# Optimization experiments

Hardware: AMD Instinct MI355X
Metric: run time of the kernel (lower is better)

Reference implementation:

```python
import jax, jax.numpy as jnp
import numpy as np
import math

B = 1024      # graphs
N = 64        # nodes per graph (padded, masked by node_mask)
BN = B * N    # total nodes
EPG = 192     # directed edges per graph
E = B * EPG


def setup_inputs() -> dict:
    key = jax.random.key(0)
    ks = jax.random.split(key, 40)

    def nrm(k, shp, s=0.02):
        return (jax.random.normal(k, shp) * s).astype(jnp.float32)

    mol_batch_x = jax.random.normal(ks[0], (BN, 19), dtype=jnp.float32)
    offs = jnp.arange(B, dtype=jnp.int32) * N
    src = jax.random.randint(ks[1], (B, EPG), 0, N, dtype=jnp.int32) + offs[:, None]
    dst = jax.random.randint(ks[2], (B, EPG), 0, N, dtype=jnp.int32) + offs[:, None]
    mol_batch_edge_index = jnp.stack([src.reshape(-1), dst.reshape(-1)], axis=0)
    mol_batch_batch = jnp.repeat(jnp.arange(B, dtype=jnp.int32), N)
    text_features = jax.random.normal(ks[3], (B, 300), dtype=jnp.float32)
    timesteps = jax.random.uniform(ks[4], (B,), minval=0.0, maxval=1000.0, dtype=jnp.float32)
    node_mask = (jax.random.uniform(ks[5], (B, N)) > 0.1).astype(jnp.float32)

    p = {
        'W_tr': nrm(ks[6], (19, 300)),   'b_tr': jnp.zeros((300,), jnp.float32),
        'W_c1': nrm(ks[7], (300, 600)),  'b_c1': jnp.zeros((600,), jnp.float32),
        'W_c2': nrm(ks[8], (600, 600)),  'b_c2': jnp.zeros((600,), jnp.float32),
        'W_c3': nrm(ks[9], (600, 600)),  'b_c3': jnp.zeros((600,), jnp.float32),
        'W_h1': nrm(ks[10], (600, 600)), 'b_h1': jnp.zeros((600,), jnp.float32),
        'W_h2': nrm(ks[11], (600, 600)), 'b_h2': jnp.zeros((600,), jnp.float32),
        'W_h3': nrm(ks[12], (600, 300)), 'b_h3': jnp.zeros((300,), jnp.float32),
        'ln_g': jnp.ones((300,), jnp.float32), 'ln_b': jnp.zeros((300,), jnp.float32),
        'W_t1': nrm(ks[13], (128, 512)), 'b_t1': jnp.zeros((512,), jnp.float32),
        'W_t2': nrm(ks[14], (512, 512)), 'b_t2': jnp.zeros((512,), jnp.float32),
        'W_e':  nrm(ks[15], (512, 3000)), 'b_e': jnp.zeros((3000,), jnp.float32),
    }
    return dict(mol_batch_x=mol_batch_x, mol_batch_edge_index=mol_batch_edge_index,
                mol_batch_batch=mol_batch_batch, text_features=text_features,
                timesteps=timesteps, node_mask=node_mask, **p)


def timestep_embedding(t, dim=128, max_period=10000.0):
    half = dim // 2
    freqs = jnp.exp(-math.log(max_period) * jnp.arange(half, dtype=jnp.float32) / half)
    args = t[:, None] * freqs[None]                 # [B, half]
    return jnp.concatenate([jnp.cos(args), jnp.sin(args)], axis=-1)  # [B, dim]


def gcn_conv(x, W, b, src, dst, num_nodes):
    # PyG GCNConv: D^{-1/2} (A + I) D^{-1/2} X W + b, edge weights 1
    h = x @ W                                             # [BN, F]
    deg = jnp.zeros((num_nodes,), h.dtype).at[dst].add(1.0) + 1.0  # in-degree + self-loop
    inv_sqrt = jax.lax.rsqrt(deg)
    coef = inv_sqrt[src] * inv_sqrt[dst]                  # [E]
    agg = jax.ops.segment_sum(h[src] * coef[:, None], dst, num_segments=num_nodes)
    return agg + h * (1.0 / deg)[:, None] + b             # self-loop norm = 1/deg


def global_mean_pool(x, batch, num_graphs):
    sums = jax.ops.segment_sum(x, batch, num_segments=num_graphs)
    cnts = jax.ops.segment_sum(jnp.ones((x.shape[0],), x.dtype), batch, num_segments=num_graphs)
    return sums / jnp.maximum(cnts, 1.0)[:, None]


def layer_norm(x, g, b, eps=1e-5):
    mu = jnp.mean(x, axis=-1, keepdims=True)
    var = jnp.mean(jnp.square(x - mu), axis=-1, keepdims=True)
    return (x - mu) * jax.lax.rsqrt(var + eps) * g + b


def reference(mol_batch_x, mol_batch_edge_index, mol_batch_batch, text_features,
              timesteps, node_mask, W_tr, b_tr, W_c1, b_c1, W_c2, b_c2, W_c3, b_c3,
              W_h1, b_h1, W_h2, b_h2, W_h3, b_h3, ln_g, ln_b,
              W_t1, b_t1, W_t2, b_t2, W_e, b_e):
    num_nodes = mol_batch_x.shape[0]
    num_graphs = node_mask.shape[0]
    src, dst = mol_batch_edge_index[0], mol_batch_edge_index[1]

    # FiLM conditioning from timestep embedding
    emb = jax.nn.relu(timestep_embedding(timesteps, 128) @ W_t1 + b_t1) @ W_t2 + b_t2  # [B,512]
    emb_out = jax.nn.relu(emb) @ W_e + b_e                                             # [B,3000]
    s1, t1 = emb_out[:, 0:600], emb_out[:, 600:1200]
    s2, t2 = emb_out[:, 1200:1800], emb_out[:, 1800:2400]
    s3, t3 = emb_out[:, 2400:2700], emb_out[:, 2700:3000]

    # node transform + mask
    x = mol_batch_x @ W_tr + b_tr                     # [BN, 300]
    x = x * node_mask.reshape(-1, 1)

    # GCN stack
    x = jax.nn.relu(gcn_conv(x, W_c1, b_c1, src, dst, num_nodes))
    x = jax.nn.relu(gcn_conv(x, W_c2, b_c2, src, dst, num_nodes))
    x = gcn_conv(x, W_c3, b_c3, src, dst, num_nodes)  # [BN, 600]

    g = global_mean_pool(x, mol_batch_batch, num_graphs)  # [B, 600]
    g = jax.nn.relu(g @ W_h1 + b_h1)
    g = g * (1.0 + s1) + t1
    g = jax.nn.relu(g @ W_h2 + b_h2)
    g = g * (1.0 + s2) + t2
    g = g @ W_h3 + b_h3                                # [B, 300]
    g = g * (1.0 + s3) + t3
    g = layer_norm(g, ln_g, ln_b)
    return (g, text_features)
```

## Files before the change

### kernel.cpp

```cpp
#include <hip/hip_runtime.h>
#include <hip/hip_bf16.h>
#include <cstdint>
#include <cstddef>

static constexpr int B   = 1024;
static constexpr int N   = 64;
static constexpr int BN  = B * N;
static constexpr int EPG = 192;
static constexpr int E   = B * EPG;
static constexpr int FP  = 608;
static constexpr int KP1 = 320;
static constexpr int PMS = 80;
static constexpr int NCONV = 2560;

typedef __hip_bfloat16 bf16;
typedef __bf16 bf16x8 __attribute__((ext_vector_type(8)));
typedef __bf16 bf16x4 __attribute__((ext_vector_type(4)));
typedef float  f32x4  __attribute__((ext_vector_type(4)));

__device__ __forceinline__ void storeC(float* p, float v) { *p = v; }
__device__ __forceinline__ void storeC(bf16* p, float v) { *p = __float2bfloat16(v); }

__device__ __forceinline__ void llds16(const void* g, void* l) {
    __builtin_amdgcn_global_load_lds(
        (const __attribute__((address_space(1))) unsigned int*)g,
        (__attribute__((address_space(3))) unsigned int*)l,
        16, 0, 0);
}

template<bool RELU, bool FILM, typename CT>
__device__ __forceinline__ void g64_tile(
    const bf16* __restrict__ A, int lda,
    const bf16* __restrict__ Bt, int ldb,
    const float* __restrict__ bias,
    CT* __restrict__ C, int ldc, int Ncap,
    const bf16* __restrict__ fS, const bf16* __restrict__ fT, int fstride,
    int K, int m0, int n0, __bf16* As, __bf16* Bs, int tid)
{
    const int lane = tid & 63;
    const int w    = tid >> 6;
    const int wn   = w * 32;
    const int l15  = lane & 15;
    const int lhi  = lane >> 4;

    f32x4 acc[4][2] = {};

    for (int k0 = 0; k0 < K; k0 += 32) {
        {
            int row = tid >> 2, kc = tid & 3;
            char* la = (char*)As + (size_t)(w * 64) * 16;
            llds16(A + (size_t)(m0 + row) * lda + k0 + kc * 8, la);
        }
        #pragma unroll
        for (int t = 0; t < 2; ++t) {
            int ci  = t * 256 + tid;
            int row = ci >> 2, kc = ci & 3;
            char* lb = (char*)Bs + (size_t)(t * 256 + w * 64) * 16;
            llds16(Bt + (size_t)(n0 + row) * ldb + k0 + kc * 8, lb);
        }
        asm volatile("s_waitcnt vmcnt(0)" ::: "memory");
        __syncthreads();

        bf16x8 af[4], bg[2];
        #pragma unroll
        for (int i = 0; i < 4; ++i)
            af[i] = *(bf16x8*)(As + (i * 16 + l15) * 32 + lhi * 8);
        #pragma unroll
        for (int j = 0; j < 2; ++j)
            bg[j] = *(bf16x8*)(Bs + (wn + j * 16 + l15) * 32 + lhi * 8);
        #pragma unroll
        for (int i = 0; i < 4; ++i)
            #pragma unroll
            for (int j = 0; j < 2; ++j)
                acc[i][j] = __builtin_amdgcn_mfma_f32_16x16x32_bf16(
                    af[i], bg[j], acc[i][j], 0, 0, 0);
        __syncthreads();
    }

    #pragma unroll
    for (int i = 0; i < 4; ++i) {
        #pragma unroll
        for (int j = 0; j < 2; ++j) {
            int col = n0 + wn + j * 16 + l15;
            if (col < Ncap) {
                float bv = bias ? bias[col] : 0.f;
                #pragma unroll
                for (int e = 0; e < 4; ++e) {
                    int row = m0 + i * 16 + lhi * 4 + e;
                    float v = acc[i][j][e] + bv;
                    if (RELU) v = fmaxf(v, 0.f);
                    if (FILM) {
                        float sv = __bfloat162float(fS[(size_t)row * fstride + col]);
                        float tv = __bfloat162float(fT[(size_t)row * fstride + col]);
                        v = v * (1.f + sv) + tv;
                    }
                    storeC(&C[(size_t)row * ldc + col], v);
                }
            }
        }
    }
}

__device__ __attribute__((noinline)) void guest_g64(
    const bf16* gA, int glda, const bf16* gBt, int gldb,
    const float* gbias, bf16* gC, int gldc, int gNcap, int gK, int gnt,
    int t, char* lds, int tid)
{
    int mt2 = t / gnt, nt2 = t % gnt;
    g64_tile<true, false, bf16>(gA, glda, gBt, gldb, gbias, gC, gldc, gNcap,
                                nullptr, nullptr, 0, gK, mt2 * 64, nt2 * 128,
                                (__bf16*)lds, (__bf16*)(lds + 4096), tid);
}

template<bool RELU, bool FILM, typename CT>
__global__ __launch_bounds__(256) void gemm64(
    const bf16* __restrict__ A, int lda,
    const bf16* __restrict__ Bt, int ldb,
    const float* __restrict__ bias,
    CT* __restrict__ C, int ldc, int Ncap,
    const bf16* __restrict__ fS, const bf16* __restrict__ fT, int fstride,
    int K)
{
    __shared__ __align__(16) __bf16 As[64 * 32];
    __shared__ __align__(16) __bf16 Bs[128 * 32];
    g64_tile<RELU, FILM, CT>(A, lda, Bt, ldb, bias, C, ldc, Ncap,
                             fS, fT, fstride, K,
                             blockIdx.x * 64, blockIdx.y * 128, As, Bs,
                             threadIdx.x);
}

__global__ __launch_bounds__(256) void k_two_gemms(
    const bf16* __restrict__ A2b, const bf16* __restrict__ Wet,
    const float* __restrict__ b_e, bf16* __restrict__ EO,
    const bf16* __restrict__ Yv, const bf16* __restrict__ Wb3,
    const float* __restrict__ b_c3, bf16* __restrict__ G0)
{
    __shared__ __align__(16) __bf16 As[64 * 32];
    __shared__ __align__(16) __bf16 Bs[128 * 32];
    int bid = blockIdx.x;
    if (bid < 384) {
        int mt = bid / 24, nt = bid % 24;
        g64_tile<false, false, bf16>(A2b, 512, Wet, 512, b_e, EO, 3000, 3000,
                                     nullptr, nullptr, 0, 512,
                                     mt * 64, nt * 128, As, Bs, threadIdx.x);
    } else {
        int t = bid - 384;
        int mt = t / 5, nt = t % 5;
        g64_tile<false, false, bf16>(Yv, FP, Wb3, FP, b_c3, G0, FP, 600,
                                     nullptr, nullptr, 0, FP,
                                     mt * 64, nt * 128, As, Bs, threadIdx.x);
    }
}

__global__ __launch_bounds__(256) void conv1_gemm(
    const bf16* __restrict__ A,
    const bf16* __restrict__ Bt,
    const float* __restrict__ bias,
    bf16* __restrict__ X1,
    const bf16* __restrict__ gA, int glda,
    const bf16* __restrict__ gBt, int gldb,
    const float* __restrict__ gbias,
    bf16* __restrict__ gC, int gldc, int gNcap, int gK, int gnt)
{
    __shared__ __align__(16) char regA[17408];
    const int tid = threadIdx.x;
    const int bid = blockIdx.x;

    if (bid >= NCONV) {
        guest_g64(gA, glda, gBt, gldb, gbias, gC, gldc, gNcap, gK, gnt,
                  bid - NCONV, regA, tid);
        return;
    }

    __bf16* As = (__bf16*)regA;
    __bf16* Bs = (__bf16*)(regA + 8192);

    const int lane = tid & 63;
    const int w    = tid >> 6;
    const int wm   = (w & 1) * 64;
    const int wn   = (w >> 1) * 64;
    const int l15  = lane & 15;
    const int lhi  = lane >> 4;

    const int lid = bid >> 3;
    const int mt  = (bid & 7) * 64 + lid / 5;
    const int nt  = lid % 5;
    const int m0  = mt * 128;
    const int n0  = nt * 128;

    f32x4 acc[4][4] = {};
    for (int k0 = 0; k0 < KP1; k0 += 32) {
        #pragma unroll
        for (int t = 0; t < 2; ++t) {
            int ci  = t * 256 + w * 64 + lane;
            int row = ci >> 2, kc = ci & 3;
            char* la = (char*)As + (size_t)(t * 256 + w * 64) * 16;
            char* lb = (char*)Bs + (size_t)(t * 256 + w * 64) * 16;
            llds16(A  + (size_t)(m0 + row) * KP1 + k0 + kc * 8, la);
            llds16(Bt + (size_t)(n0 + row) * KP1 + k0 + kc * 8, lb);
        }
        asm volatile("s_waitcnt vmcnt(0)" ::: "memory");
        __syncthreads();

        bf16x8 af[4], bg[4];
        #pragma unroll
        for (int i = 0; i < 4; ++i)
            af[i] = *(bf16x8*)(As + (wm + i * 16 + l15) * 32 + lhi * 8);
        #pragma unroll
        for (int j = 0; j < 4; ++j)
            bg[j] = *(bf16x8*)(Bs + (wn + j * 16 + l15) * 32 + lhi * 8);
        #pragma unroll
        for (int i = 0; i < 4; ++i)
            #pragma unroll
            for (int j = 0; j < 4; ++j)
                acc[i][j] = __builtin_amdgcn_mfma_f32_16x16x32_bf16(
                    af[i], bg[j], acc[i][j], 0, 0, 0);
        __syncthreads();
    }

    #pragma unroll
    for (int i = 0; i < 4; ++i)
        #pragma unroll
        for (int j = 0; j < 4; ++j) {
            int col = n0 + wn + j * 16 + l15;
            if (col < FP) {
                float bv = (col < 600) ? bias[col] : 0.f;
                #pragma unroll
                for (int e = 0; e < 4; ++e) {
                    int row = m0 + wm + i * 16 + lhi * 4 + e;
                    float v = fmaxf(acc[i][j][e] + bv, 0.f);
                    X1[(size_t)row * FP + col] = __float2bfloat16(v);
                }
            }
        }
}

__global__ __launch_bounds__(256) void conv_fused_q(
    const bf16* __restrict__ A, int lda, int K,
    const bf16* __restrict__ Bt, int ldb,
    const bf16* __restrict__ Pmg,
    const float* __restrict__ bias,
    const float* __restrict__ qv,
    bf16* __restrict__ Y,
    const bf16* __restrict__ gA, int glda,
    const bf16* __restrict__ gBt, int gldb,
    const float* __restrict__ gbias,
    bf16* __restrict__ gC, int gldc, int gNcap, int gK, int gnt)
{
    __shared__ __align__(16) char regA[17408];
    __shared__ __align__(16) __bf16 Pm[128 * PMS];
    __shared__ float s_q[128];

    const int tid = threadIdx.x;
    const int bid = blockIdx.x;

    if (bid >= NCONV) {
        guest_g64(gA, glda, gBt, gldb, gbias, gC, gldc, gNcap, gK, gnt,
                  bid - NCONV, regA, tid);
        return;
    }

    __bf16* As = (__bf16*)regA;
    __bf16* Bs = (__bf16*)(regA + 8192);
    __bf16* Ts = (__bf16*)regA;

    const int lane = tid & 63;
    const int w    = tid >> 6;
    const int wm   = (w & 1) * 64;
    const int wn   = (w >> 1) * 64;
    const int l15  = lane & 15;
    const int lhi  = lane >> 4;

    const int lid = bid >> 3;
    const int mt  = (bid & 7) * 64 + lid / 5;
    const int nt  = lid % 5;
    const int m0  = mt * 128;
    const int n0  = nt * 128;

    #pragma unroll
    for (int i = 0; i < 5; ++i) {
        int cbase = w * 320 + i * 64;
        llds16(Pmg + (size_t)mt * (128 * PMS) + (size_t)(cbase + lane) * 8,
               (char*)Pm + (size_t)cbase * 16);
    }
    if (tid < 128) s_q[tid] = qv[mt * 128 + tid];

    f32x4 acc[4][4] = {};
    for (int k0 = 0; k0 < K; k0 += 32) {
        #pragma unroll
        for (int t = 0; t < 2; ++t) {
            int ci  = t * 256 + w * 64 + lane;
            int row = ci >> 2, kc = ci & 3;
            char* la = (char*)As + (size_t)(t * 256 + w * 64) * 16;
            char* lb = (char*)Bs + (size_t)(t * 256 + w * 64) * 16;
            llds16(A  + (size_t)(m0 + row) * lda + k0 + kc * 8, la);
            llds16(Bt + (size_t)(n0 + row) * ldb + k0 + kc * 8, lb);
        }
        asm volatile("s_waitcnt vmcnt(0)" ::: "memory");
        __syncthreads();

        bf16x8 af[4], bg[4];
        #pragma unroll
        for (int i = 0; i < 4; ++i)
            af[i] = *(bf16x8*)(As + (wm + i * 16 + l15) * 32 + lhi * 8);
        #pragma unroll
        for (int j = 0; j < 4; ++j)
            bg[j] = *(bf16x8*)(Bs + (wn + j * 16 + l15) * 32 + lhi * 8);
        #pragma unroll
        for (int i = 0; i < 4; ++i)
            #pragma unroll
            for (int j = 0; j < 4; ++j)
                acc[i][j] = __builtin_amdgcn_mfma_f32_16x16x32_bf16(
                    af[i], bg[j], acc[i][j], 0, 0, 0);
        __syncthreads();
    }

    const int g  = w & 1;
    const int nb = w >> 1;
    #pragma unroll
    for (int h = 0; h < 2; ++h) {
        if (wn == h * 64) {
            #pragma unroll
            for (int i = 0; i < 4; ++i)
                #pragma unroll
                for (int j = 0; j < 4; ++j) {
                    int c_local = j * 16 + l15;
                    int rbase   = wm + i * 16 + lhi * 4;
                    bf16x4 pk;
                    #pragma unroll
                    for (int e = 0; e < 4; ++e) pk[e] = (__bf16)acc[i][j][e];
                    *(bf16x4*)(Ts + c_local * 136 + rbase) = pk;
                }
        }
        __syncthreads();

        f32x4 acc2[4][2] = {};
        #pragma unroll
        for (int k0 = 0; k0 < 64; k0 += 32) {
            bf16x8 pa[4], hb[2];
            #pragma unroll
            for (int i = 0; i < 4; ++i)
                pa[i] = *(bf16x8*)(Pm + (g * 64 + i * 16 + l15) * PMS + k0 + lhi * 8);
            #pragma unroll
            for (int j = 0; j < 2; ++j)
                hb[j] = *(bf16x8*)(Ts + (nb * 32 + j * 16 + l15) * 136
                                      + g * 64 + k0 + lhi * 8);
            #pragma unroll
            for (int i = 0; i < 4; ++i)
                #pragma unroll
                for (int j = 0; j < 2; ++j)
                    acc2[i][j] = __builtin_amdgcn_mfma_f32_16x16x32_bf16(
                        pa[i], hb[j], acc2[i][j], 0, 0, 0);
        }
        #pragma unroll
        for (int j = 0; j < 2; ++j) {
            int col = n0 + h * 64 + nb * 32 + j * 16 + l15;
            float bv = (col < 600) ? bias[col] : 0.f;
            float yp = 0.f;
            #pragma unroll
            for (int i = 0; i < 4; ++i)
                #pragma unroll
                for (int e = 0; e < 4; ++e) {
                    float v = fmaxf(acc2[i][j][e] + bv, 0.f);
                    yp += s_q[g * 64 + i * 16 + lhi * 4 + e] * v;
                }
            yp += __shfl_xor(yp, 16, 64);
            yp += __shfl_xor(yp, 32, 64);
            if (lhi == 0 && col < FP)
                Y[(size_t)(mt * 2 + g) * FP + col] = __float2bfloat16(yp);
        }
        __syncthreads();
    }
}

struct WtJob  { const float* src; bf16* dst; int Ksrc, Nsrc, Kp, Np, blk0; };
struct PrepArgs {
    WtJob j[9];
    int nwt, te0, pp0, xtr0;
    const int*   ei;
    const float* ts;
    const float* xin; const float* Wtr; const float* btr; const float* mask;
    bf16* TE; bf16* Pmg; float* qv; bf16* PX0;
};

__global__ __launch_bounds__(256) void k_prep(PrepArgs a)
{
    __shared__ __align__(16) char sm[35840];
    const int bx  = blockIdx.x;
    const int tid = threadIdx.x;

    if (bx < a.nwt) {
        int ji = 0;
        while (ji < 8 && bx >= a.j[ji + 1].blk0) ++ji;
        WtJob jb = a.j[ji];
        int t  = bx - jb.blk0;
        int kt = (jb.Kp + 63) >> 6;
        int ti = t % kt, tj = t / kt;
        int kg0 = ti * 64, ng0 = tj * 64;
        float (*T)[65] = (float(*)[65])sm;
        #pragma unroll 4
        for (int r = 0; r < 16; ++r) {
            int kl = (tid >> 6) + r * 4, nl = tid & 63;
            int kg = kg0 + kl, ng = ng0 + nl;
            T[kl][nl] = (kg < jb.Ksrc && ng < jb.Nsrc)
                        ? jb.src[(size_t)kg * jb.Nsrc + ng] : 0.f;
        }
        __syncthreads();
        #pragma unroll 4
        for (int r = 0; r < 16; ++r) {
            int nl = (tid >> 6) + r * 4, kl = tid & 63;
            int ng = ng0 + nl, kg = kg0 + kl;
            if (ng < jb.Np && kg < jb.Kp)
                jb.dst[(size_t)ng * jb.Kp + kg] = __float2bfloat16(T[kl][nl]);
        }
    } else if (bx < a.pp0) {
        int idx = (bx - a.te0) * 256 + tid;
        int b = idx >> 7, jj = idx & 127;
        float tt = a.ts[b];
        int h = jj & 63;
        float freq = expf(-9.210340371976184f * (float)h / 64.f);
        float ang = tt * freq;
        a.TE[idx] = __float2bfloat16((jj < 64) ? cosf(ang) : sinf(ang));
    } else if (bx < a.xtr0) {
        int pr = bx - a.pp0;
        float* Pf   = (float*)sm;
        int*   cnt  = (int*)(sm + 32768);
        float* sQ   = (float*)(sm + 33280);
        float* sI   = (float*)(sm + 33792);
        float* sIvd = (float*)(sm + 34304);

        for (int idx = tid; idx < 8192; idx += 256) Pf[idx] = 0.f;
        if (tid < 128) cnt[tid] = 0;
        __syncthreads();
        for (int e = tid; e < 2 * EPG; e += 256) {
            int g  = (e >= EPG);
            int eg = (2 * pr + g) * EPG + (e - g * EPG);
            int ld = (a.ei[E + eg] & 63) + g * 64;
            atomicAdd(&cnt[ld], 1);
        }
        __syncthreads();
        if (tid < 128) {
            float d = (float)cnt[tid] + 1.0f;
            float iv = 1.f / d;
            sIvd[tid] = iv;
            sI[tid]   = rsqrtf(d);
            sQ[tid]   = iv;
        }
        __syncthreads();
        for (int e = tid; e < 2 * EPG; e += 256) {
            int g   = (e >= EPG);
            int eg  = (2 * pr + g) * EPG + (e - g * EPG);
            int lsl = a.ei[eg] & 63;
            int ldl = a.ei[E + eg] & 63;
            float cf = sI[g * 64 + lsl] * sI[g * 64 + ldl];
            atomicAdd(&Pf[(g * 64 + ldl) * 64 + lsl], cf);
            atomicAdd(&sQ[g * 64 + lsl], cf);
        }
        __syncthreads();
        if (tid < 128) {
            Pf[tid * 64 + (tid & 63)] += sIvd[tid];
            a.qv[pr * 128 + tid] = sQ[tid] * (1.f / 64.f);
        }
        __syncthreads();
        for (int idx = tid; idx < 128 * PMS; idx += 256) {
            int r = idx / PMS, k = idx - r * PMS;
            float v = (k < 64) ? Pf[r * 64 + k] : 0.f;
            a.Pmg[(size_t)pr * (128 * PMS) + idx] = __float2bfloat16(v);
        }
    } else {
        int g = bx - a.xtr0;
        float* Pf  = (float*)sm;
        float* Ws  = (float*)sm;
        float* xm  = (float*)(sm + 23104);
        float* xa  = (float*)(sm + 28224);
        float* isqv= (float*)(sm + 33344);
        float* ivdv= (float*)(sm + 33600);
        int*   cnt = (int*)  (sm + 33856);
        float* sb  = (float*)(sm + 34112);

        for (int idx = tid; idx < 4096; idx += 256) Pf[idx] = 0.f;
        if (tid < 64) cnt[tid] = 0;
        __syncthreads();
        for (int e = tid; e < EPG; e += 256)
            atomicAdd(&cnt[a.ei[E + g * EPG + e] & 63], 1);
        __syncthreads();
        if (tid < 64) {
            float d = (float)cnt[tid] + 1.0f;
            ivdv[tid] = 1.f / d;
            isqv[tid] = rsqrtf(d);
        }
        __syncthreads();
        for (int e = tid; e < EPG; e += 256) {
            int ls = a.ei[g * EPG + e] & 63;
            int ld = a.ei[E + g * EPG + e] & 63;
            atomicAdd(&Pf[ld * 64 + ls], isqv[ls] * isqv[ld]);
        }
        for (int idx = tid; idx < 64 * 20; idx += 256) {
            int n = idx / 20, j = idx - n * 20;
            float mv = a.mask[g * 64 + n];
            xm[idx] = (j < 19) ? mv * a.xin[(size_t)(g * 64 + n) * 19 + j] : mv;
        }
        __syncthreads();
        if (tid < 64) Pf[tid * 64 + tid] += ivdv[tid];
        __syncthreads();
        for (int idx = tid; idx < 64 * 20; idx += 256) {
            int r = idx / 20, j = idx - r * 20;
            float s = 0.f;
            #pragma unroll 8
            for (int s2 = 0; s2 < 64; ++s2)
                s += Pf[r * 64 + s2] * xm[s2 * 20 + j];
            xa[idx] = s;
        }
        __syncthreads();
        for (int idx = tid; idx < 19 * 304; idx += 256) {
            int k = idx / 304, c = idx - k * 304;
            Ws[idx] = (c < 300) ? a.Wtr[k * 300 + c] : 0.f;
        }
        for (int c = tid; c < 304; c += 256)
            sb[c] = (c < 300) ? a.btr[c] : 0.f;
        __syncthreads();
        int n  = tid >> 2;
        int c0 = tid & 3;
        float ba = xa[n * 20 + 19];
        for (int c = c0; c < 304; c += 4) {
            float acc = ba * sb[c];
            #pragma unroll
            for (int k = 0; k < 19; ++k)
                acc += xa[n * 20 + k] * Ws[k * 304 + c];
            a.PX0[(size_t)(g * 64 + n) * KP1 + c] = __float2bfloat16(acc);
        }
        bf16x8 z = {};
        for (int idx = tid; idx < 64 * 2; idx += 256) {
            int nn = idx >> 1, jv = idx & 1;
            *(bf16x8*)((__bf16*)a.PX0 + (size_t)(g * 64 + nn) * KP1 + 304 + jv * 8) = z;
        }
    }
}

__global__ __launch_bounds__(256) void k_ln_copy(const float* __restrict__ G,
                                                 const float* __restrict__ lg,
                                                 const float* __restrict__ lb,
                                                 const float* __restrict__ text,
                                                 float* __restrict__ out)
{
    int r = blockIdx.x;
    int tid = threadIdx.x;
    __shared__ float red[4];
    __shared__ float smu, svar;

    float v0 = (tid < 300) ? G[r * 300 + tid] : 0.f;
    float v1 = (tid + 256 < 300) ? G[r * 300 + tid + 256] : 0.f;
    float s = v0 + v1;
    #pragma unroll
    for (int o = 32; o > 0; o >>= 1) s += __shfl_down(s, o, 64);
    if ((tid & 63) == 0) red[tid >> 6] = s;
    __syncthreads();
    if (tid == 0) smu = (red[0] + red[1] + red[2] + red[3]) * (1.f / 300.f);
    __syncthreads();
    float mu = smu;
    float d0 = (tid < 300) ? v0 - mu : 0.f;
    float d1 = (tid + 256 < 300) ? v1 - mu : 0.f;
    s = d0 * d0 + d1 * d1;
    #pragma unroll
    for (int o = 32; o > 0; o >>= 1) s += __shfl_down(s, o, 64);
    if ((tid & 63) == 0) red[tid >> 6] = s;
    __syncthreads();
    if (tid == 0) svar = (red[0] + red[1] + red[2] + red[3]) * (1.f / 300.f);
    __syncthreads();
    float rstd = rsqrtf(svar + 1e-5f);
    if (tid < 300)
        out[r * 300 + tid] = d0 * rstd * lg[tid] + lb[tid];
    if (tid + 256 < 300)
        out[r * 300 + tid + 256] = d1 * rstd * lg[tid + 256] + lb[tid + 256];
    float* o2 = out + (size_t)B * 300;
    for (int c = tid; c < 300; c += 256)
        o2[(size_t)r * 300 + c] = text[(size_t)r * 300 + c];
}

extern "C" void kernel_launch(void* const* d_in, const int* in_sizes, int n_in,
                              void* d_out, int out_size, void* d_ws, size_t ws_size,
                              hipStream_t stream)
{
    const float* x_in  = (const float*)d_in[0];
    const int*   ei    = (const int*)d_in[1];
    const float* text  = (const float*)d_in[3];
    const float* tst   = (const float*)d_in[4];
    const float* mask  = (const float*)d_in[5];
    const float* W_tr  = (const float*)d_in[6];
    const float* b_tr  = (const float*)d_in[7];
    const float* W_c1  = (const float*)d_in[8];
    const float* b_c1  = (const float*)d_in[9];
    const float* W_c2  = (const float*)d_in[10];
    const float* b_c2  = (const float*)d_in[11];
    const float* W_c3  = (const float*)d_in[12];
    const float* b_c3  = (const float*)d_in[13];
    const float* W_h1  = (const float*)d_in[14];
    const float* b_h1  = (const float*)d_in[15];
    const float* W_h2  = (const float*)d_in[16];
    const float* b_h2  = (const float*)d_in[17];
    const float* W_h3  = (const float*)d_in[18];
    const float* b_h3  = (const float*)d_in[19];
    const float* ln_g  = (const float*)d_in[20];
    const float* ln_b  = (const float*)d_in[21];
    const float* W_t1  = (const float*)d_in[22];
    const float* b_t1  = (const float*)d_in[23];
    const float* W_t2  = (const float*)d_in[24];
    const float* b_t2  = (const float*)d_in[25];
    const float* W_e   = (const float*)d_in[26];
    const float* b_e   = (const float*)d_in[27];

    char* w = (char*)d_ws;
    size_t off = 0;
    auto carve = [&](size_t bytes) {
        void* p = w + off;
        off += (bytes + 255) & ~(size_t)255;
        return p;
    };
    bf16*  PX0    = (bf16*) carve((size_t)BN * KP1 * 2);
    bf16*  X1     = (bf16*) carve((size_t)BN * FP * 2);
    bf16*  Wb1    = (bf16*) carve((size_t)640 * KP1 * 2);
    bf16*  Wb2    = (bf16*) carve((size_t)640 * FP * 2);
    bf16*  Wb3    = (bf16*) carve((size_t)640 * FP * 2);
    bf16*  Wt1t   = (bf16*) carve((size_t)512 * 128 * 2);
    bf16*  Wt2t   = (bf16*) carve((size_t)512 * 512 * 2);
    bf16*  Wet    = (bf16*) carve((size_t)3072 * 512 * 2);
    bf16*  Wh1t   = (bf16*) carve((size_t)640 * FP * 2);
    bf16*  Wh2t   = (bf16*) carve((size_t)640 * FP * 2);
    bf16*  Wh3t   = (bf16*) carve((size_t)384 * FP * 2);
    bf16*  TE     = (bf16*) carve((size_t)B * 128 * 2);
    bf16*  A1b    = (bf16*) carve((size_t)B * 512 * 2);
    bf16*  A2b    = (bf16*) carve((size_t)B * 512 * 2);
    bf16*  EO     = (bf16*) carve((size_t)B * 3000 * 2);
    bf16*  Yv     = (bf16*) carve((size_t)B * FP * 2);
    bf16*  G0     = (bf16*) carve((size_t)B * FP * 2);
    bf16*  G1     = (bf16*) carve((size_t)B * FP * 2);
    bf16*  G2     = (bf16*) carve((size_t)B * FP * 2);
    float* G3     = (float*)carve((size_t)B * 300 * 4);
    bf16*  Pmg    = (bf16*) carve((size_t)512 * 128 * PMS * 2);
    float* qv     = (float*)carve((size_t)BN * 4);
    (void)ws_size; (void)in_sizes; (void)n_in; (void)out_size;

    float* out = (float*)d_out;

    PrepArgs pa;
    struct JD { const float* s; bf16* d; int Ks, Ns, Kp, Np; };
    JD jd[9] = {
        { W_c1, Wb1,  300, 600,  KP1, 640 },
        { W_c2, Wb2,  600, 600,  FP,  640 },
        { W_c3, Wb3,  600, 600,  FP,  640 },
        { W_t1, Wt1t, 128, 512,  128, 512 },
        { W_t2, Wt2t, 512, 512,  512, 512 },
        { W_e,  Wet,  512, 3000, 512, 3072 },
        { W_h1, Wh1t, 600, 600,  FP,  640 },
        { W_h2, Wh2t, 600, 600,  FP,  640 },
        { W_h3, Wh3t, 600, 300,  FP,  384 },
    };
    int cum = 0;
    for (int i = 0; i < 9; ++i) {
        int kt = (jd[i].Kp + 63) >> 6, nt = (jd[i].Np + 63) >> 6;
        pa.j[i] = { jd[i].s, jd[i].d, jd[i].Ks, jd[i].Ns, jd[i].Kp, jd[i].Np, cum };
        cum += kt * nt;
    }
    pa.nwt  = cum;
    pa.te0  = cum;       cum += (B * 128) / 256;
    pa.pp0  = cum;       cum += B / 2;
    pa.xtr0 = cum;       cum += B;
    pa.ei = ei; pa.ts = tst;
    pa.xin = x_in; pa.Wtr = W_tr; pa.btr = b_tr; pa.mask = mask;
    pa.TE = TE; pa.Pmg = Pmg; pa.qv = qv; pa.PX0 = PX0;
    k_prep<<<cum, 256, 0, stream>>>(pa);

    conv1_gemm<<<NCONV + 64, 256, 0, stream>>>(
        PX0, Wb1, b_c1, X1,
        TE, 128, Wt1t, 128, b_t1, A1b, 512, 512, 128, 4);

    conv_fused_q<<<NCONV + 64, 256, 0, stream>>>(
        X1, FP, FP, Wb2, FP, Pmg, b_c2, qv, Yv,
        A1b, 512, Wt2t, 512, b_t2, A2b, 512, 512, 512, 4);

    k_two_gemms<<<464, 256, 0, stream>>>(A2b, Wet, b_e, EO, Yv, Wb3, b_c3, G0);

    gemm64<true, true, bf16><<<dim3(16, 5), 256, 0, stream>>>(
        G0, FP, Wh1t, FP, b_h1, G1, FP, 600, EO + 0, EO + 600, 3000, FP);
    gemm64<true, true, bf16><<<dim3(16, 5), 256, 0, stream>>>(
        G1, FP, Wh2t, FP, b_h2, G2, FP, 600, EO + 1200, EO + 1800, 3000, FP);
    gemm64<false, true, float><<<dim3(16, 3), 256, 0, stream>>>(
        G2, FP, Wh3t, FP, b_h3, G3, 300, 300, EO + 2400, EO + 2700, 3000, FP);

    k_ln_copy<<<B, 256, 0, stream>>>(G3, ln_g, ln_b, text, out);
}
```

Baseline: 366.6 us.

## Double GEMM K-step to 64 with XOR-swizzled LDS layout, pad features to 640

All MFMA GEMM tiles now stage 64-wide K slices per iteration instead of 32, halving the number of barrier/wait rounds, and use an XOR swizzle on the 16-byte chunk index to avoid LDS bank conflicts on fragment reads. The padded feature width FP goes from 608 to 640 so K is a multiple of 64, with epilogues writing zeros into the padded columns. Late-stage buffers are aliased over the dead PX0 region to cut workspace footprint. LDS usage per block doubles, which may reduce occupancy.

```diff
diff --git a/kernel.cpp b/kernel.cpp
--- a/kernel.cpp
+++ b/kernel.cpp
@@ -8,9 +8,9 @@
 static constexpr int BN  = B * N;
 static constexpr int EPG = 192;
 static constexpr int E   = B * EPG;
-static constexpr int FP  = 608;
+static constexpr int FP  = 640;
 static constexpr int KP1 = 320;
-static constexpr int PMS = 80;
+static constexpr int PMS = 72;
 static constexpr int NCONV = 2560;
 
 typedef __hip_bfloat16 bf16;
@@ -28,12 +28,13 @@
         16, 0, 0);
 }
 
+
 template<bool RELU, bool FILM, typename CT>
 __device__ __forceinline__ void g64_tile(
     const bf16* __restrict__ A, int lda,
     const bf16* __restrict__ Bt, int ldb,
     const float* __restrict__ bias,
-    CT* __restrict__ C, int ldc, int Ncap,
+    CT* __restrict__ C, int ldc, int Ncap, int Npad,
     const bf16* __restrict__ fS, const bf16* __restrict__ fT, int fstride,
     int K, int m0, int n0, __bf16* As, __bf16* Bs, int tid)
 {
@@ -42,38 +43,47 @@
     const int wn   = w * 32;
     const int l15  = lane & 15;
     const int lhi  = lane >> 4;
+    const int sx   = l15 & 7;
 
     f32x4 acc[4][2] = {};
 
-    for (int k0 = 0; k0 < K; k0 += 32) {
-        {
-            int row = tid >> 2, kc = tid & 3;
-            char* la = (char*)As + (size_t)(w * 64) * 16;
-            llds16(A + (size_t)(m0 + row) * lda + k0 + kc * 8, la);
-        }
+    for (int k0 = 0; k0 < K; k0 += 64) {
         #pragma unroll
         for (int t = 0; t < 2; ++t) {
             int ci  = t * 256 + tid;
-            int row = ci >> 2, kc = ci & 3;
-            char* lb = (char*)Bs + (size_t)(t * 256 + w * 64) * 16;
-            llds16(Bt + (size_t)(n0 + row) * ldb + k0 + kc * 8, lb);
+            int row = ci >> 3;
+            int kc  = (ci & 7) ^ (row & 7);
+            llds16(A + (size_t)(m0 + row) * lda + k0 + kc * 8,
+                   (char*)As + (size_t)(t * 256 + w * 64) * 16);
+        }
+        #pragma unroll
+        for (int t = 0; t < 4; ++t) {
+            int ci  = t * 256 + tid;
+            int row = ci >> 3;
+            int kc  = (ci & 7) ^ (row & 7);
+            llds16(Bt + (size_t)(n0 + row) * ldb + k0 + kc * 8,
+                   (char*)Bs + (size_t)(t * 256 + w * 64) * 16);
         }
         asm volatile("s_waitcnt vmcnt(0)" ::: "memory");
         __syncthreads();
 
-        bf16x8 af[4], bg[2];
-        #pragma unroll
-        for (int i = 0; i < 4; ++i)
-            af[i] = *(bf16x8*)(As + (i * 16 + l15) * 32 + lhi * 8);
-        #pragma unroll
-        for (int j = 0; j < 2; ++j)
-            bg[j] = *(bf16x8*)(Bs + (wn + j * 16 + l15) * 32 + lhi * 8);
-        #pragma unroll
-        for (int i = 0; i < 4; ++i)
+        #pragma unroll
+        for (int ks = 0; ks < 2; ++ks) {
+            const int co = ((ks * 4 + lhi) ^ sx) << 3;
+            bf16x8 af[4], bg[2];
+            #pragma unroll
+            for (int i = 0; i < 4; ++i)
+                af[i] = *(bf16x8*)(As + (i * 16 + l15) * 64 + co);
             #pragma unroll
             for (int j = 0; j < 2; ++j)
-                acc[i][j] = __builtin_amdgcn_mfma_f32_16x16x32_bf16(
-                    af[i], bg[j], acc[i][j], 0, 0, 0);
+                bg[j] = *(bf16x8*)(Bs + (wn + j * 16 + l15) * 64 + co);
+            #pragma unroll
+            for (int i = 0; i < 4; ++i)
+                #pragma unroll
+                for (int j = 0; j < 2; ++j)
+                    acc[i][j] = __builtin_amdgcn_mfma_f32_16x16x32_bf16(
+                        af[i], bg[j], acc[i][j], 0, 0, 0);
+        }
         __syncthreads();
     }
 
@@ -82,17 +92,21 @@
         #pragma unroll
         for (int j = 0; j < 2; ++j) {
             int col = n0 + wn + j * 16 + l15;
-            if (col < Ncap) {
-                float bv = bias ? bias[col] : 0.f;
+            if (col < Npad) {
                 #pragma unroll
                 for (int e = 0; e < 4; ++e) {
                     int row = m0 + i * 16 + lhi * 4 + e;
-                    float v = acc[i][j][e] + bv;
-                    if (RELU) v = fmaxf(v, 0.f);
-                    if (FILM) {
-                        float sv = __bfloat162float(fS[(size_t)row * fstride + col]);
-                        float tv = __bfloat162float(fT[(size_t)row * fstride + col]);
-                        v = v * (1.f + sv) + tv;
+                    float v;
+                    if (col < Ncap) {
+                        v = acc[i][j][e] + (bias ? bias[col] : 0.f);
+                        if (RELU) v = fmaxf(v, 0.f);
+                        if (FILM) {
+                            float sv = __bfloat162float(fS[(size_t)row * fstride + col]);
+                            float tv = __bfloat162float(fT[(size_t)row * fstride + col]);
+                            v = v * (1.f + sv) + tv;
+                        }
+                    } else {
+                        v = 0.f;
                     }
                     storeC(&C[(size_t)row * ldc + col], v);
                 }
@@ -108,8 +122,9 @@
 {
     int mt2 = t / gnt, nt2 = t % gnt;
     g64_tile<true, false, bf16>(gA, glda, gBt, gldb, gbias, gC, gldc, gNcap,
-                                nullptr, nullptr, 0, gK, mt2 * 64, nt2 * 128,
-                                (__bf16*)lds, (__bf16*)(lds + 4096), tid);
+                                gNcap, nullptr, nullptr, 0, gK,
+                                mt2 * 64, nt2 * 128,
+                                (__bf16*)lds, (__bf16*)(lds + 8192), tid);
 }
 
 template<bool RELU, bool FILM, typename CT>
@@ -117,13 +132,13 @@
     const bf16* __restrict__ A, int lda,
     const bf16* __restrict__ Bt, int ldb,
     const float* __restrict__ bias,
-    CT* __restrict__ C, int ldc, int Ncap,
+    CT* __restrict__ C, int ldc, int Ncap, int Npad,
     const bf16* __restrict__ fS, const bf16* __restrict__ fT, int fstride,
     int K)
 {
-    __shared__ __align__(16) __bf16 As[64 * 32];
-    __shared__ __align__(16) __bf16 Bs[128 * 32];
-    g64_tile<RELU, FILM, CT>(A, lda, Bt, ldb, bias, C, ldc, Ncap,
+    __shared__ __align__(16) __bf16 As[64 * 64];
+    __shared__ __align__(16) __bf16 Bs[128 * 64];
+    g64_tile<RELU, FILM, CT>(A, lda, Bt, ldb, bias, C, ldc, Ncap, Npad,
                              fS, fT, fstride, K,
                              blockIdx.x * 64, blockIdx.y * 128, As, Bs,
                              threadIdx.x);
@@ -135,19 +150,19 @@
     const bf16* __restrict__ Yv, const bf16* __restrict__ Wb3,
     const float* __restrict__ b_c3, bf16* __restrict__ G0)
 {
-    __shared__ __align__(16) __bf16 As[64 * 32];
-    __shared__ __align__(16) __bf16 Bs[128 * 32];
+    __shared__ __align__(16) __bf16 As[64 * 64];
+    __shared__ __align__(16) __bf16 Bs[128 * 64];
     int bid = blockIdx.x;
     if (bid < 384) {
         int mt = bid / 24, nt = bid % 24;
         g64_tile<false, false, bf16>(A2b, 512, Wet, 512, b_e, EO, 3000, 3000,
-                                     nullptr, nullptr, 0, 512,
+                                     3000, nullptr, nullptr, 0, 512,
                                      mt * 64, nt * 128, As, Bs, threadIdx.x);
     } else {
         int t = bid - 384;
         int mt = t / 5, nt = t % 5;
         g64_tile<false, false, bf16>(Yv, FP, Wb3, FP, b_c3, G0, FP, 600,
-                                     nullptr, nullptr, 0, FP,
+                                     FP, nullptr, nullptr, 0, FP,
                                      mt * 64, nt * 128, As, Bs, threadIdx.x);
     }
 }
@@ -162,7 +177,7 @@
     const float* __restrict__ gbias,
     bf16* __restrict__ gC, int gldc, int gNcap, int gK, int gnt)
 {
-    __shared__ __align__(16) char regA[17408];
+    __shared__ __align__(16) char regA[32768];
     const int tid = threadIdx.x;
     const int bid = blockIdx.x;
 
@@ -173,7 +188,7 @@
     }
 
     __bf16* As = (__bf16*)regA;
-    __bf16* Bs = (__bf16*)(regA + 8192);
+    __bf16* Bs = (__bf16*)(regA + 16384);
 
     const int lane = tid & 63;
     const int w    = tid >> 6;
@@ -181,6 +196,7 @@
     const int wn   = (w >> 1) * 64;
     const int l15  = lane & 15;
     const int lhi  = lane >> 4;
+    const int sx   = l15 & 7;
 
     const int lid = bid >> 3;
     const int mt  = (bid & 7) * 64 + lid / 5;
@@ -189,11 +205,12 @@
     const int n0  = nt * 128;
 
     f32x4 acc[4][4] = {};
-    for (int k0 = 0; k0 < KP1; k0 += 32) {
-        #pragma unroll
-        for (int t = 0; t < 2; ++t) {
-            int ci  = t * 256 + w * 64 + lane;
-            int row = ci >> 2, kc = ci & 3;
+    for (int k0 = 0; k0 < KP1; k0 += 64) {
+        #pragma unroll
+        for (int t = 0; t < 4; ++t) {
+            int ci  = t * 256 + tid;
+            int row = ci >> 3;
+            int kc  = (ci & 7) ^ (row & 7);
             char* la = (char*)As + (size_t)(t * 256 + w * 64) * 16;
             char* lb = (char*)Bs + (size_t)(t * 256 + w * 64) * 16;
             llds16(A  + (size_t)(m0 + row) * KP1 + k0 + kc * 8, la);
@@ -202,19 +219,23 @@
         asm volatile("s_waitcnt vmcnt(0)" ::: "memory");
         __syncthreads();
 
-        bf16x8 af[4], bg[4];
-        #pragma unroll
-        for (int i = 0; i < 4; ++i)
-            af[i] = *(bf16x8*)(As + (wm + i * 16 + l15) * 32 + lhi * 8);
-        #pragma unroll
-        for (int j = 0; j < 4; ++j)
-            bg[j] = *(bf16x8*)(Bs + (wn + j * 16 + l15) * 32 + lhi * 8);
-        #pragma unroll
-        for (int i = 0; i < 4; ++i)
+        #pragma unroll
+        for (int ks = 0; ks < 2; ++ks) {
+            const int co = ((ks * 4 + lhi) ^ sx) << 3;
+            bf16x8 af[4], bg[4];
+            #pragma unroll
+            for (int i = 0; i < 4; ++i)
+                af[i] = *(bf16x8*)(As + (wm + i * 16 + l15) * 64 + co);
             #pragma unroll
             for (int j = 0; j < 4; ++j)
-                acc[i][j] = __builtin_amdgcn_mfma_f32_16x16x32_bf16(
-                    af[i], bg[j], acc[i][j], 0, 0, 0);
+                bg[j] = *(bf16x8*)(Bs + (wn + j * 16 + l15) * 64 + co);
+            #pragma unroll
+            for (int i = 0; i < 4; ++i)
+                #pragma unroll
+                for (int j = 0; j < 4; ++j)
+                    acc[i][j] = __builtin_amdgcn_mfma_f32_16x16x32_bf16(
+                        af[i], bg[j], acc[i][j], 0, 0, 0);
+        }
         __syncthreads();
     }
 
@@ -247,7 +268,7 @@
     const float* __restrict__ gbias,
     bf16* __restrict__ gC, int gldc, int gNcap, int gK, int gnt)
 {
-    __shared__ __align__(16) char regA[17408];
+    __shared__ __align__(16) char regA[32768];
     __shared__ __align__(16) __bf16 Pm[128 * PMS];
     __shared__ float s_q[128];
 
@@ -261,7 +282,7 @@
     }
 
     __bf16* As = (__bf16*)regA;
-    __bf16* Bs = (__bf16*)(regA + 8192);
+    __bf16* Bs = (__bf16*)(regA + 16384);
     __bf16* Ts = (__bf16*)regA;
 
     const int lane = tid & 63;
@@ -270,6 +291,7 @@
     const int wn   = (w >> 1) * 64;
     const int l15  = lane & 15;
     const int lhi  = lane >> 4;
+    const int sx   = l15 & 7;
 
     const int lid = bid >> 3;
     const int mt  = (bid & 7) * 64 + lid / 5;
@@ -278,19 +300,21 @@
     const int n0  = nt * 128;
 
     #pragma unroll
-    for (int i = 0; i < 5; ++i) {
-        int cbase = w * 320 + i * 64;
-        llds16(Pmg + (size_t)mt * (128 * PMS) + (size_t)(cbase + lane) * 8,
-               (char*)Pm + (size_t)cbase * 16);
-    }
+    for (int i = 0; i < 4; ++i)
+        llds16(Pmg + (size_t)mt * (128 * PMS) + (size_t)(i * 256 + tid) * 8,
+               (char*)Pm + (size_t)(i * 256 + w * 64) * 16);
+    if (w < 2)
+        llds16(Pmg + (size_t)mt * (128 * PMS) + (size_t)(1024 + w * 64 + lane) * 8,
+               (char*)Pm + (size_t)(1024 + w * 64) * 16);
     if (tid < 128) s_q[tid] = qv[mt * 128 + tid];
 
     f32x4 acc[4][4] = {};
-    for (int k0 = 0; k0 < K; k0 += 32) {
-        #pragma unroll
-        for (int t = 0; t < 2; ++t) {
-            int ci  = t * 256 + w * 64 + lane;
-            int row = ci >> 2, kc = ci & 3;
+    for (int k0 = 0; k0 < K; k0 += 64) {
+        #pragma unroll
+        for (int t = 0; t < 4; ++t) {
+            int ci  = t * 256 + tid;
+            int row = ci >> 3;
+            int kc  = (ci & 7) ^ (row & 7);
             char* la = (char*)As + (size_t)(t * 256 + w * 64) * 16;
             char* lb = (char*)Bs + (size_t)(t * 256 + w * 64) * 16;
             llds16(A  + (size_t)(m0 + row) * lda + k0 + kc * 8, la);
@@ -299,19 +323,23 @@
         asm volatile("s_waitcnt vmcnt(0)" ::: "memory");
         __syncthreads();
 
-        bf16x8 af[4], bg[4];
-        #pragma unroll
-        for (int i = 0; i < 4; ++i)
-            af[i] = *(bf16x8*)(As + (wm + i * 16 + l15) * 32 + lhi * 8);
-        #pragma unroll
-        for (int j = 0; j < 4; ++j)
-            bg[j] = *(bf16x8*)(Bs + (wn + j * 16 + l15) * 32 + lhi * 8);
-        #pragma unroll
-        for (int i = 0; i < 4; ++i)
+        #pragma unroll
+        for (int ks = 0; ks < 2; ++ks) {
+            const int co = ((ks * 4 + lhi) ^ sx) << 3;
+            bf16x8 af[4], bg[4];
+            #pragma unroll
+            for (int i = 0; i < 4; ++i)
+                af[i] = *(bf16x8*)(As + (wm + i * 16 + l15) * 64 + co);
             #pragma unroll
             for (int j = 0; j < 4; ++j)
-                acc[i][j] = __builtin_amdgcn_mfma_f32_16x16x32_bf16(
-                    af[i], bg[j], acc[i][j], 0, 0, 0);
+                bg[j] = *(bf16x8*)(Bs + (wn + j * 16 + l15) * 64 + co);
+            #pragma unroll
+            for (int i = 0; i < 4; ++i)
+                #pragma unroll
+                for (int j = 0; j < 4; ++j)
+                    acc[i][j] = __builtin_amdgcn_mfma_f32_16x16x32_bf16(
+                        af[i], bg[j], acc[i][j], 0, 0, 0);
+        }
         __syncthreads();
     }
 
@@ -629,15 +657,22 @@
     bf16*  Wh3t   = (bf16*) carve((size_t)384 * FP * 2);
     bf16*  TE     = (bf16*) carve((size_t)B * 128 * 2);
     bf16*  A1b    = (bf16*) carve((size_t)B * 512 * 2);
-    bf16*  A2b    = (bf16*) carve((size_t)B * 512 * 2);
-    bf16*  EO     = (bf16*) carve((size_t)B * 3000 * 2);
-    bf16*  Yv     = (bf16*) carve((size_t)B * FP * 2);
-    bf16*  G0     = (bf16*) carve((size_t)B * FP * 2);
-    bf16*  G1     = (bf16*) carve((size_t)B * FP * 2);
-    bf16*  G2     = (bf16*) carve((size_t)B * FP * 2);
-    float* G3     = (float*)carve((size_t)B * 300 * 4);
     bf16*  Pmg    = (bf16*) carve((size_t)512 * 128 * PMS * 2);
     float* qv     = (float*)carve((size_t)BN * 4);
+    char* ali = (char*)PX0;
+    size_t aoff = 0;
+    auto carve2 = [&](size_t bytes) {
+        void* p = ali + aoff;
+        aoff += (bytes + 255) & ~(size_t)255;
+        return p;
+    };
+    bf16*  A2b    = (bf16*) carve2((size_t)B * 512 * 2);
+    bf16*  EO     = (bf16*) carve2((size_t)B * 3000 * 2);
+    bf16*  Yv     = (bf16*) carve2((size_t)B * FP * 2);
+    bf16*  G0     = (bf16*) carve2((size_t)B * FP * 2);
+    bf16*  G1     = (bf16*) carve2((size_t)B * FP * 2);
+    bf16*  G2     = (bf16*) carve2((size_t)B * FP * 2);
+    float* G3     = (float*)carve2((size_t)B * 300 * 4);
     (void)ws_size; (void)in_sizes; (void)n_in; (void)out_size;
 
     float* out = (float*)d_out;
@@ -681,11 +716,11 @@
     k_two_gemms<<<464, 256, 0, stream>>>(A2b, Wet, b_e, EO, Yv, Wb3, b_c3, G0);
 
     gemm64<true, true, bf16><<<dim3(16, 5), 256, 0, stream>>>(
-        G0, FP, Wh1t, FP, b_h1, G1, FP, 600, EO + 0, EO + 600, 3000, FP);
+        G0, FP, Wh1t, FP, b_h1, G1, FP, 600, FP, EO + 0, EO + 600, 3000, FP);
     gemm64<true, true, bf16><<<dim3(16, 5), 256, 0, stream>>>(
-        G1, FP, Wh2t, FP, b_h2, G2, FP, 600, EO + 1200, EO + 1800, 3000, FP);
+        G1, FP, Wh2t, FP, b_h2, G2, FP, 600, FP, EO + 1200, EO + 1800, 3000, FP);
     gemm64<false, true, float><<<dim3(16, 3), 256, 0, stream>>>(
-        G2, FP, Wh3t, FP, b_h3, G3, 300, 300, EO + 2400, EO + 2700, 3000, FP);
+        G2, FP, Wh3t, FP, b_h3, G3, 300, 300, 300, EO + 2400, EO + 2700, 3000, FP);
 
     k_ln_copy<<<B, 256, 0, stream>>>(G3, ln_g, ln_b, text, out);
 }
```

Measured after the change: 393.8 us. 1.07x slower.

## Double-buffer GEMM LDS tiles with XOR swizzle and defer propagation-matrix load

Applied to the files above, without the earlier changes.

All GEMM main loops (g64 tiles, conv1, conv_fused_q) now use two LDS buffers, so the next K-slice's global-to-LDS loads are issued before the current slice's MFMAs instead of serialising load, wait and compute. The K-chunk index is XOR-swizzled by row on both store and read to cut LDS bank conflicts. The per-graph propagation matrix is now loaded during the last K iteration, overlapped with compute, and its padded stride drops from 80 to 72. The cost is roughly double the LDS per block, and conv kernels get launch_bounds(256,4), which may lower occupancy or force register pressure.

```diff
diff --git a/kernel.cpp b/kernel.cpp
--- a/kernel.cpp
+++ b/kernel.cpp
@@ -10,7 +10,7 @@
 static constexpr int E   = B * EPG;
 static constexpr int FP  = 608;
 static constexpr int KP1 = 320;
-static constexpr int PMS = 80;
+static constexpr int PMS = 72;
 static constexpr int NCONV = 2560;
 
 typedef __hip_bfloat16 bf16;
@@ -27,6 +27,7 @@
         (__attribute__((address_space(3))) unsigned int*)l,
         16, 0, 0);
 }
+
 
 template<bool RELU, bool FILM, typename CT>
 __device__ __forceinline__ void g64_tile(
@@ -35,45 +36,58 @@
     const float* __restrict__ bias,
     CT* __restrict__ C, int ldc, int Ncap,
     const bf16* __restrict__ fS, const bf16* __restrict__ fT, int fstride,
-    int K, int m0, int n0, __bf16* As, __bf16* Bs, int tid)
+    int K, int m0, int n0, char* lds, int tid)
 {
     const int lane = tid & 63;
     const int w    = tid >> 6;
     const int wn   = w * 32;
     const int l15  = lane & 15;
     const int lhi  = lane >> 4;
-
-    f32x4 acc[4][2] = {};
-
-    for (int k0 = 0; k0 < K; k0 += 32) {
+    const int co   = (lhi ^ ((l15 >> 1) & 3)) << 3;
+    const int nk   = K >> 5;
+
+    auto stage = [&](int k0, char* buf) {
         {
-            int row = tid >> 2, kc = tid & 3;
-            char* la = (char*)As + (size_t)(w * 64) * 16;
-            llds16(A + (size_t)(m0 + row) * lda + k0 + kc * 8, la);
+            int row = tid >> 2;
+            int kc  = (tid & 3) ^ ((row >> 1) & 3);
+            llds16(A + (size_t)(m0 + row) * lda + k0 + kc * 8,
+                   buf + (size_t)(w * 64) * 16);
         }
         #pragma unroll
         for (int t = 0; t < 2; ++t) {
             int ci  = t * 256 + tid;
-            int row = ci >> 2, kc = ci & 3;
-            char* lb = (char*)Bs + (size_t)(t * 256 + w * 64) * 16;
-            llds16(Bt + (size_t)(n0 + row) * ldb + k0 + kc * 8, lb);
-        }
-        asm volatile("s_waitcnt vmcnt(0)" ::: "memory");
-        __syncthreads();
-
+            int row = ci >> 2;
+            int kc  = (ci & 3) ^ ((row >> 1) & 3);
+            llds16(Bt + (size_t)(n0 + row) * ldb + k0 + kc * 8,
+                   buf + 4096 + (size_t)(t * 256 + w * 64) * 16);
+        }
+    };
+
+    f32x4 acc[4][2] = {};
+    stage(0, lds);
+    asm volatile("s_waitcnt vmcnt(0)" ::: "memory");
+    __syncthreads();
+
+    for (int k = 0; k < nk; ++k) {
+        if (k + 1 < nk) stage((k + 1) << 5, lds + ((k + 1) & 1) * 12288);
+
+        __bf16* As = (__bf16*)(lds + (k & 1) * 12288);
+        __bf16* Bs = As + 2048;
         bf16x8 af[4], bg[2];
         #pragma unroll
         for (int i = 0; i < 4; ++i)
-            af[i] = *(bf16x8*)(As + (i * 16 + l15) * 32 + lhi * 8);
+            af[i] = *(bf16x8*)(As + (i * 16 + l15) * 32 + co);
         #pragma unroll
         for (int j = 0; j < 2; ++j)
-            bg[j] = *(bf16x8*)(Bs + (wn + j * 16 + l15) * 32 + lhi * 8);
+            bg[j] = *(bf16x8*)(Bs + (wn + j * 16 + l15) * 32 + co);
         #pragma unroll
         for (int i = 0; i < 4; ++i)
             #pragma unroll
             for (int j = 0; j < 2; ++j)
                 acc[i][j] = __builtin_amdgcn_mfma_f32_16x16x32_bf16(
                     af[i], bg[j], acc[i][j], 0, 0, 0);
+
+        asm volatile("s_waitcnt vmcnt(0)" ::: "memory");
         __syncthreads();
     }
 
@@ -109,7 +123,7 @@
     int mt2 = t / gnt, nt2 = t % gnt;
     g64_tile<true, false, bf16>(gA, glda, gBt, gldb, gbias, gC, gldc, gNcap,
                                 nullptr, nullptr, 0, gK, mt2 * 64, nt2 * 128,
-                                (__bf16*)lds, (__bf16*)(lds + 4096), tid);
+                                lds, tid);
 }
 
 template<bool RELU, bool FILM, typename CT>
@@ -121,11 +135,10 @@
     const bf16* __restrict__ fS, const bf16* __restrict__ fT, int fstride,
     int K)
 {
-    __shared__ __align__(16) __bf16 As[64 * 32];
-    __shared__ __align__(16) __bf16 Bs[128 * 32];
+    __shared__ __align__(16) char lds[24576];
     g64_tile<RELU, FILM, CT>(A, lda, Bt, ldb, bias, C, ldc, Ncap,
                              fS, fT, fstride, K,
-                             blockIdx.x * 64, blockIdx.y * 128, As, Bs,
+                             blockIdx.x * 64, blockIdx.y * 128, lds,
                              threadIdx.x);
 }
 
@@ -135,24 +148,23 @@
     const bf16* __restrict__ Yv, const bf16* __restrict__ Wb3,
     const float* __restrict__ b_c3, bf16* __restrict__ G0)
 {
-    __shared__ __align__(16) __bf16 As[64 * 32];
-    __shared__ __align__(16) __bf16 Bs[128 * 32];
+    __shared__ __align__(16) char lds[24576];
     int bid = blockIdx.x;
     if (bid < 384) {
         int mt = bid / 24, nt = bid % 24;
         g64_tile<false, false, bf16>(A2b, 512, Wet, 512, b_e, EO, 3000, 3000,
                                      nullptr, nullptr, 0, 512,
-                                     mt * 64, nt * 128, As, Bs, threadIdx.x);
+                                     mt * 64, nt * 128, lds, threadIdx.x);
     } else {
         int t = bid - 384;
         int mt = t / 5, nt = t % 5;
         g64_tile<false, false, bf16>(Yv, FP, Wb3, FP, b_c3, G0, FP, 600,
                                      nullptr, nullptr, 0, FP,
-                                     mt * 64, nt * 128, As, Bs, threadIdx.x);
-    }
-}
-
-__global__ __launch_bounds__(256) void conv1_gemm(
+                                     mt * 64, nt * 128, lds, threadIdx.x);
+    }
+}
+
+__global__ __launch_bounds__(256, 4) void conv1_gemm(
     const bf16* __restrict__ A,
     const bf16* __restrict__ Bt,
     const float* __restrict__ bias,
@@ -162,7 +174,7 @@
     const float* __restrict__ gbias,
     bf16* __restrict__ gC, int gldc, int gNcap, int gK, int gnt)
 {
-    __shared__ __align__(16) char regA[17408];
+    __shared__ __align__(16) char regA[32768];
     const int tid = threadIdx.x;
     const int bid = blockIdx.x;
 
@@ -171,9 +183,6 @@
                   bid - NCONV, regA, tid);
         return;
     }
-
-    __bf16* As = (__bf16*)regA;
-    __bf16* Bs = (__bf16*)(regA + 8192);
 
     const int lane = tid & 63;
     const int w    = tid >> 6;
@@ -181,6 +190,7 @@
     const int wn   = (w >> 1) * 64;
     const int l15  = lane & 15;
     const int lhi  = lane >> 4;
+    const int co   = (lhi ^ ((l15 >> 1) & 3)) << 3;
 
     const int lid = bid >> 3;
     const int mt  = (bid & 7) * 64 + lid / 5;
@@ -188,33 +198,45 @@
     const int m0  = mt * 128;
     const int n0  = nt * 128;
 
+    auto stage = [&](int k0, char* buf) {
+        #pragma unroll
+        for (int t = 0; t < 2; ++t) {
+            int ci  = t * 256 + tid;
+            int row = ci >> 2;
+            int kc  = (ci & 3) ^ ((row >> 1) & 3);
+            llds16(A  + (size_t)(m0 + row) * KP1 + k0 + kc * 8,
+                   buf + (size_t)(t * 256 + w * 64) * 16);
+            llds16(Bt + (size_t)(n0 + row) * KP1 + k0 + kc * 8,
+                   buf + 8192 + (size_t)(t * 256 + w * 64) * 16);
+        }
+    };
+
+    constexpr int nk = KP1 / 32;
     f32x4 acc[4][4] = {};
-    for (int k0 = 0; k0 < KP1; k0 += 32) {
-        #pragma unroll
-        for (int t = 0; t < 2; ++t) {
-            int ci  = t * 256 + w * 64 + lane;
-            int row = ci >> 2, kc = ci & 3;
-            char* la = (char*)As + (size_t)(t * 256 + w * 64) * 16;
-            char* lb = (char*)Bs + (size_t)(t * 256 + w * 64) * 16;
-            llds16(A  + (size_t)(m0 + row) * KP1 + k0 + kc * 8, la);
-            llds16(Bt + (size_t)(n0 + row) * KP1 + k0 + kc * 8, lb);
-        }
-        asm volatile("s_waitcnt vmcnt(0)" ::: "memory");
-        __syncthreads();
-
+    stage(0, regA);
+    asm volatile("s_waitcnt vmcnt(0)" ::: "memory");
+    __syncthreads();
+
+    for (int k = 0; k < nk; ++k) {
+        if (k + 1 < nk) stage((k + 1) << 5, regA + ((k + 1) & 1) * 16384);
+
+        __bf16* As = (__bf16*)(regA + (k & 1) * 16384);
+        __bf16* Bs = As + 4096;
         bf16x8 af[4], bg[4];
         #pragma unroll
         for (int i = 0; i < 4; ++i)
-            af[i] = *(bf16x8*)(As + (wm + i * 16 + l15) * 32 + lhi * 8);
+            af[i] = *(bf16x8*)(As + (wm + i * 16 + l15) * 32 + co);
         #pragma unroll
         for (int j = 0; j < 4; ++j)
-            bg[j] = *(bf16x8*)(Bs + (wn + j * 16 + l15) * 32 + lhi * 8);
+            bg[j] = *(bf16x8*)(Bs + (wn + j * 16 + l15) * 32 + co);
         #pragma unroll
         for (int i = 0; i < 4; ++i)
             #pragma unroll
             for (int j = 0; j < 4; ++j)
                 acc[i][j] = __builtin_amdgcn_mfma_f32_16x16x32_bf16(
                     af[i], bg[j], acc[i][j], 0, 0, 0);
+
+        asm volatile("s_waitcnt vmcnt(0)" ::: "memory");
         __syncthreads();
     }
 
@@ -235,7 +257,7 @@
         }
 }
 
-__global__ __launch_bounds__(256) void conv_fused_q(
+__global__ __launch_bounds__(256, 4) void conv_fused_q(
     const bf16* __restrict__ A, int lda, int K,
     const bf16* __restrict__ Bt, int ldb,
     const bf16* __restrict__ Pmg,
@@ -247,8 +269,7 @@
     const float* __restrict__ gbias,
     bf16* __restrict__ gC, int gldc, int gNcap, int gK, int gnt)
 {
-    __shared__ __align__(16) char regA[17408];
-    __shared__ __align__(16) __bf16 Pm[128 * PMS];
+    __shared__ __align__(16) char regA[35840];
     __shared__ float s_q[128];
 
     const int tid = threadIdx.x;
@@ -260,9 +281,8 @@
         return;
     }
 
-    __bf16* As = (__bf16*)regA;
-    __bf16* Bs = (__bf16*)(regA + 8192);
     __bf16* Ts = (__bf16*)regA;
+    __bf16* Pm = (__bf16*)(regA + 17408);
 
     const int lane = tid & 63;
     const int w    = tid >> 6;
@@ -270,6 +290,7 @@
     const int wn   = (w >> 1) * 64;
     const int l15  = lane & 15;
     const int lhi  = lane >> 4;
+    const int co   = (lhi ^ ((l15 >> 1) & 3)) << 3;
 
     const int lid = bid >> 3;
     const int mt  = (bid & 7) * 64 + lid / 5;
@@ -277,41 +298,57 @@
     const int m0  = mt * 128;
     const int n0  = nt * 128;
 
-    #pragma unroll
-    for (int i = 0; i < 5; ++i) {
-        int cbase = w * 320 + i * 64;
-        llds16(Pmg + (size_t)mt * (128 * PMS) + (size_t)(cbase + lane) * 8,
-               (char*)Pm + (size_t)cbase * 16);
-    }
     if (tid < 128) s_q[tid] = qv[mt * 128 + tid];
 
+    auto stage = [&](int k0, char* buf) {
+        #pragma unroll
+        for (int t = 0; t < 2; ++t) {
+            int ci  = t * 256 + tid;
+            int row = ci >> 2;
+            int kc  = (ci & 3) ^ ((row >> 1) & 3);
+            llds16(A  + (size_t)(m0 + row) * lda + k0 + kc * 8,
+                   buf + (size_t)(t * 256 + w * 64) * 16);
+            llds16(Bt + (size_t)(n0 + row) * ldb + k0 + kc * 8,
+                   buf + 8192 + (size_t)(t * 256 + w * 64) * 16);
+        }
+    };
+
+    const int nk = K >> 5;
     f32x4 acc[4][4] = {};
-    for (int k0 = 0; k0 < K; k0 += 32) {
-        #pragma unroll
-        for (int t = 0; t < 2; ++t) {
-            int ci  = t * 256 + w * 64 + lane;
-            int row = ci >> 2, kc = ci & 3;
-            char* la = (char*)As + (size_t)(t * 256 + w * 64) * 16;
-            char* lb = (char*)Bs + (size_t)(t * 256 + w * 64) * 16;
-            llds16(A  + (size_t)(m0 + row) * lda + k0 + kc * 8, la);
-            llds16(Bt + (size_t)(n0 + row) * ldb + k0 + kc * 8, lb);
-        }
-        asm volatile("s_waitcnt vmcnt(0)" ::: "memory");
-        __syncthreads();
-
+    stage(0, regA);
+    asm volatile("s_waitcnt vmcnt(0)" ::: "memory");
+    __syncthreads();
+
+    for (int k = 0; k < nk; ++k) {
+        if (k + 1 < nk) {
+            stage((k + 1) << 5, regA + ((k + 1) & 1) * 16384);
+        } else {
+            #pragma unroll
+            for (int i = 0; i < 4; ++i)
+                llds16(Pmg + (size_t)mt * (128 * PMS) + (size_t)(i * 256 + tid) * 8,
+                       (char*)Pm + (size_t)(i * 256 + w * 64) * 16);
+            if (w < 2)
+                llds16(Pmg + (size_t)mt * (128 * PMS) + (size_t)(1024 + w * 64 + lane) * 8,
+                       (char*)Pm + (size_t)(1024 + w * 64) * 16);
+        }
+
+        __bf16* As = (__bf16*)(regA + (k & 1) * 16384);
+        __bf16* Bs = As + 4096;
         bf16x8 af[4], bg[4];
         #pragma unroll
         for (int i = 0; i < 4; ++i)
-            af[i] = *(bf16x8*)(As + (wm + i * 16 + l15) * 32 + lhi * 8);
+            af[i] = *(bf16x8*)(As + (wm + i * 16 + l15) * 32 + co);
         #pragma unroll
         for (int j = 0; j < 4; ++j)
-            bg[j] = *(bf16x8*)(Bs + (wn + j * 16 + l15) * 32 + lhi * 8);
+            bg[j] = *(bf16x8*)(Bs + (wn + j * 16 + l15) * 32 + co);
         #pragma unroll
         for (int i = 0; i < 4; ++i)
             #pragma unroll
             for (int j = 0; j < 4; ++j)
                 acc[i][j] = __builtin_amdgcn_mfma_f32_16x16x32_bf16(
                     af[i], bg[j], acc[i][j], 0, 0, 0);
+
+        asm volatile("s_waitcnt vmcnt(0)" ::: "memory");
         __syncthreads();
     }
 
```

Result: faster. 341.5 us (-6.9%).
